# Kernel tuning notes

Measured on AMD Instinct MI355X. Metric: run time of the kernel, lower is better.

The kernel has to match this reference:

```python
import jax, jax.numpy as jnp
import numpy as np

NUM_EMBEDDINGS = 1024
EMBEDDING_DIM = 64


def setup_inputs() -> dict:
    key = jax.random.key(0)
    k1, k2 = jax.random.split(key)
    z = jax.random.normal(k1, (64, 32, 32, EMBEDDING_DIM), dtype=jnp.float32)
    # torch init: uniform_(-1/num_embeddings, 1/num_embeddings)
    lim = 1.0 / NUM_EMBEDDINGS
    codebook = jax.random.uniform(
        k2, (NUM_EMBEDDINGS, EMBEDDING_DIM), dtype=jnp.float32,
        minval=-lim, maxval=lim)
    return {"z": z, "codebook": codebook}


def reference(z, codebook):
    # z: [..., D]; codebook: [K, D]
    z_flat = z.reshape(-1, z.shape[-1])                      # [N, D]
    # ||z||^2 - 2 z.e + ||e||^2  -> [N, K]
    distances = (
        jnp.sum(z_flat ** 2, axis=1, keepdims=True)
        - 2.0 * jnp.einsum("nd,kd->nk", z_flat, codebook)
        + jnp.sum(codebook ** 2, axis=1)
    )
    min_indices = jnp.argmin(distances, axis=1)              # [N]
    z_q = jnp.take(codebook, min_indices, axis=0).reshape(z.shape)
    return z_q, min_indices
```

## Files before the change

### kernel.cpp

```cpp
#include <hip/hip_runtime.h>
#include <hip/hip_bf16.h>
#include <math.h>


#define D      64
#define K      1024
#define BLOCK  256

typedef _Float16 half8_t __attribute__((ext_vector_type(8)));
typedef float    floatx4 __attribute__((ext_vector_type(4)));

#define WS_CN_OFF    0
#define WS_EF_OFF    4096

__device__ __forceinline__ float np_sumsq64_p(const float* __restrict__ x) {
    float r[8];
    {
        float4 v0 = *(const float4*)(x);
        float4 v1 = *(const float4*)(x + 4);
        r[0] = __fmul_rn(v0.x, v0.x); r[1] = __fmul_rn(v0.y, v0.y);
        r[2] = __fmul_rn(v0.z, v0.z); r[3] = __fmul_rn(v0.w, v0.w);
        r[4] = __fmul_rn(v1.x, v1.x); r[5] = __fmul_rn(v1.y, v1.y);
        r[6] = __fmul_rn(v1.z, v1.z); r[7] = __fmul_rn(v1.w, v1.w);
    }
#pragma unroll
    for (int i = 8; i < 64; i += 8) {
        float4 v0 = *(const float4*)(x + i);
        float4 v1 = *(const float4*)(x + i + 4);
        r[0] = __fadd_rn(r[0], __fmul_rn(v0.x, v0.x));
        r[1] = __fadd_rn(r[1], __fmul_rn(v0.y, v0.y));
        r[2] = __fadd_rn(r[2], __fmul_rn(v0.z, v0.z));
        r[3] = __fadd_rn(r[3], __fmul_rn(v0.w, v0.w));
        r[4] = __fadd_rn(r[4], __fmul_rn(v1.x, v1.x));
        r[5] = __fadd_rn(r[5], __fmul_rn(v1.y, v1.y));
        r[6] = __fadd_rn(r[6], __fmul_rn(v1.z, v1.z));
        r[7] = __fadd_rn(r[7], __fmul_rn(v1.w, v1.w));
    }
    return __fadd_rn(__fadd_rn(__fadd_rn(r[0], r[1]), __fadd_rn(r[2], r[3])),
                     __fadd_rn(__fadd_rn(r[4], r[5]), __fadd_rn(r[6], r[7])));
}

__global__ void vq_pre(const float* __restrict__ cb, float* __restrict__ cn,
                       _Float16* __restrict__ ef) {
    const int k = blockIdx.x * 64 + threadIdx.x;
    if (k >= K) return;
    cn[k] = np_sumsq64_p(cb + (long)k * D);
    const int t = k >> 6, ct = (k >> 4) & 3, l16 = k & 15;
#pragma unroll
    for (int ch = 0; ch < 2; ++ch)
#pragma unroll
        for (int quad = 0; quad < 4; ++quad) {
            const float* p = cb + (long)k * D + ch * 32 + quad * 8;
            half8_t h1, h2;
#pragma unroll
            for (int j = 0; j < 8; ++j) {
                float x10 = __fmul_rn(p[j], 1024.0f);
                _Float16 g1 = (_Float16)x10;
                h1[j] = g1;
                h2[j] = (_Float16)(__fmul_rn(__fsub_rn(x10, (float)g1), 2048.0f));
            }
            const int base = t * 8192 + ct * 2048 + 128 * quad + 8 * l16;
            *(half8_t*)(ef + base + 512 * (ch))       = h1;
            *(half8_t*)(ef + base + 512 * (2 + ch))   = h2;
        }
}

__global__ __launch_bounds__(BLOCK, 2) void vq_main(
    const float* __restrict__ z, const float* __restrict__ cb,
    const _Float16* __restrict__ ef, const float* __restrict__ cn,
    float* __restrict__ zq, float* __restrict__ idx_out) {
    __shared__ __align__(16) float zf[128 * 68];
    __shared__ float sS[128];
    __shared__ float sCn[K];
    __shared__ int   sBi[128];

    const int tid  = threadIdx.x;
    const int lane = tid & 63;
    const int wv   = tid >> 6;
    const int quad = lane >> 4;
    const int l16  = lane & 15;
    const long rowbase = (long)blockIdx.x * 128;

    const float4* gz = (const float4*)(z + rowbase * D);
#pragma unroll
    for (int i = 0; i < 8; ++i) {
        int idx4 = i * BLOCK + tid;
        int r = idx4 >> 4, j = idx4 & 15;
        *(float4*)(zf + r * 68 + j * 4) = gz[idx4];
    }
#pragma unroll
    for (int i = 0; i < 4; ++i) sCn[i * 256 + tid] = cn[i * 256 + tid];
    __syncthreads();

    if (tid < 128) sS[tid] = np_sumsq64_p(zf + tid * 68);

    half8_t a1[2][2], a2[2][2];
#pragma unroll
    for (int rt = 0; rt < 2; ++rt) {
        const int row = wv * 32 + rt * 16 + l16;
#pragma unroll
        for (int ch = 0; ch < 2; ++ch) {
            const float* p = zf + row * 68 + ch * 32 + quad * 8;
            float4 f0 = *(const float4*)(p);
            float4 f1 = *(const float4*)(p + 4);
            float xs[8] = {f0.x, f0.y, f0.z, f0.w, f1.x, f1.y, f1.z, f1.w};
#pragma unroll
            for (int j = 0; j < 8; ++j) {
                _Float16 h1 = (_Float16)xs[j];
                a1[rt][ch][j] = h1;
                a2[rt][ch][j] =
                    (_Float16)(__fmul_rn(__fsub_rn(xs[j], (float)h1), 2048.0f));
            }
        }
    }
    __syncthreads();

    float myS[2][4];
#pragma unroll
    for (int rt = 0; rt < 2; ++rt)
#pragma unroll
        for (int r = 0; r < 4; ++r)
            myS[rt][r] = sS[wv * 32 + rt * 16 + quad * 4 + r];

    float bv[2][4];
    int   bi[2][4];
#pragma unroll
    for (int rt = 0; rt < 2; ++rt)
#pragma unroll
        for (int r = 0; r < 4; ++r) { bv[rt][r] = INFINITY; bi[rt][r] = 0; }

    const char* eb = (const char*)ef + 16 * lane;
    const floatx4 Z4g = {0.f, 0.f, 0.f, 0.f};

#define LOADG(b1_, b2_, g_) do {                                              \
        const char* p_ = eb + (size_t)(g_) * 4096;                            \
        b1_[0] = *(const half8_t*)(p_);                                       \
        b1_[1] = *(const half8_t*)(p_ + 1024);                                \
        b2_[0] = *(const half8_t*)(p_ + 2048);                                \
        b2_[1] = *(const half8_t*)(p_ + 3072);                                \
    } while (0)

#define COMPUTE(b1_, b2_, g_) do {                                            \
        const int   kg_  = (g_) * 16 + l16;                                   \
        const float cnv_ = sCn[kg_];                                          \
        floatx4 aM0, aM1, aC0, aC1;                                           \
        aM0 = __builtin_amdgcn_mfma_f32_16x16x32_f16(a1[0][0], b1_[0], Z4g, 0, 0, 0); \
        aM1 = __builtin_amdgcn_mfma_f32_16x16x32_f16(a1[1][0], b1_[0], Z4g, 0, 0, 0); \
        aM0 = __builtin_amdgcn_mfma_f32_16x16x32_f16(a1[0][1], b1_[1], aM0, 0, 0, 0); \
        aM1 = __builtin_amdgcn_mfma_f32_16x16x32_f16(a1[1][1], b1_[1], aM1, 0, 0, 0); \
        aC0 = __builtin_amdgcn_mfma_f32_16x16x32_f16(a1[0][0], b2_[0], Z4g, 0, 0, 0); \
        aC1 = __builtin_amdgcn_mfma_f32_16x16x32_f16(a1[1][0], b2_[0], Z4g, 0, 0, 0); \
        aC0 = __builtin_amdgcn_mfma_f32_16x16x32_f16(a1[0][1], b2_[1], aC0, 0, 0, 0); \
        aC1 = __builtin_amdgcn_mfma_f32_16x16x32_f16(a1[1][1], b2_[1], aC1, 0, 0, 0); \
        aC0 = __builtin_amdgcn_mfma_f32_16x16x32_f16(a2[0][0], b1_[0], aC0, 0, 0, 0); \
        aC1 = __builtin_amdgcn_mfma_f32_16x16x32_f16(a2[1][0], b1_[0], aC1, 0, 0, 0); \
        aC0 = __builtin_amdgcn_mfma_f32_16x16x32_f16(a2[0][1], b1_[1], aC0, 0, 0, 0); \
        aC1 = __builtin_amdgcn_mfma_f32_16x16x32_f16(a2[1][1], b1_[1], aC1, 0, 0, 0); \
        _Pragma("unroll")                                                     \
        for (int r = 0; r < 4; ++r) {                                         \
            float ds0 = fmaf(aC0[r], 0x1p-11f, aM0[r]);                       \
            float d0  = __fadd_rn(__fsub_rn(myS[0][r],                        \
                            __fmul_rn(ds0, 0x1p-9f)), cnv_);                  \
            if (d0 < bv[0][r]) { bv[0][r] = d0; bi[0][r] = kg_; }             \
            float ds1 = fmaf(aC1[r], 0x1p-11f, aM1[r]);                       \
            float d1  = __fadd_rn(__fsub_rn(myS[1][r],                        \
                            __fmul_rn(ds1, 0x1p-9f)), cnv_);                  \
            if (d1 < bv[1][r]) { bv[1][r] = d1; bi[1][r] = kg_; }             \
        }                                                                     \
    } while (0)

    half8_t b1A[2], b2A[2], b1B[2], b2B[2], b1C[2], b2C[2];
    LOADG(b1A, b2A, 0);
    LOADG(b1B, b2B, 1);
    for (int g = 0; g < 63; g += 3) {
        LOADG(b1C, b2C, g + 2);
        COMPUTE(b1A, b2A, g);
        if (g + 3 < 64) LOADG(b1A, b2A, g + 3);
        COMPUTE(b1B, b2B, g + 1);
        if (g + 4 < 64) LOADG(b1B, b2B, g + 4);
        COMPUTE(b1C, b2C, g + 2);
    }
    COMPUTE(b1A, b2A, 63);

#undef LOADG
#undef COMPUTE

#pragma unroll
    for (int rt = 0; rt < 2; ++rt)
#pragma unroll
        for (int r = 0; r < 4; ++r) {
            float v = bv[rt][r];
            int   x = bi[rt][r];
#pragma unroll
            for (int off = 1; off <= 8; off <<= 1) {
                float ov = __shfl_xor(v, off);
                int   ox = __shfl_xor(x, off);
                if (ov < v || (ov == v && ox < x)) { v = ov; x = ox; }
            }
            if (l16 == 0) {
                const int rl = wv * 32 + rt * 16 + quad * 4 + r;
                sBi[rl] = x;
                idx_out[rowbase + rl] = (float)x;
            }
        }
    __syncthreads();

    const float4* cb4 = (const float4*)cb;
    float4* zq4 = (float4*)(zq + rowbase * D);
#pragma unroll
    for (int i = 0; i < 8; ++i) {
        int idx4 = i * BLOCK + tid;
        int r = idx4 >> 4, j = idx4 & 15;
        zq4[idx4] = cb4[(long)sBi[r] * 16 + j];
    }
}

extern "C" void kernel_launch(void* const* d_in, const int* in_sizes, int n_in,
                              void* d_out, int out_size, void* d_ws, size_t ws_size,
                              hipStream_t stream) {
    const float* z  = (const float*)d_in[0];
    const float* cb = (const float*)d_in[1];

    const int n_rows = in_sizes[0] / D;
    float* zq      = (float*)d_out;
    float* idx_out = zq + (long)n_rows * D;

    float*    ws_cn = (float*)((char*)d_ws + WS_CN_OFF);
    _Float16* ws_ef = (_Float16*)((char*)d_ws + WS_EF_OFF);

    vq_pre<<<K / 64, 64, 0, stream>>>(cb, ws_cn, ws_ef);
    vq_main<<<n_rows / 128, BLOCK, 0, stream>>>(z, cb, ws_ef, ws_cn, zq, idx_out);
}
```

Before: 102.1 us.

## Prefetch codebook before z staging, shorten MFMA chains, prescale norms

Issues the first two codebook fragment loads before staging z into shared memory, so that global latency overlaps the prologue. Splits the correction MFMA accumulation into two independent chains (aC and aD), which shortens dependency depth. Prescales the z and codebook norms by 512 so one multiply per distance drops out. Parallelises the row sum-of-squares across 256 threads with a shuffle, and prefetches the codebook norm from shared memory alongside the fragments. Costs are higher register pressure and slightly different float rounding in the distance terms.

New measurement: 103.0 us. About the same (+0.8%).

```diff
diff --git a/kernel.cpp b/kernel.cpp
--- a/kernel.cpp
+++ b/kernel.cpp
@@ -81,58 +81,9 @@
     const int l16  = lane & 15;
     const long rowbase = (long)blockIdx.x * 128;
 
-    const float4* gz = (const float4*)(z + rowbase * D);
-#pragma unroll
-    for (int i = 0; i < 8; ++i) {
-        int idx4 = i * BLOCK + tid;
-        int r = idx4 >> 4, j = idx4 & 15;
-        *(float4*)(zf + r * 68 + j * 4) = gz[idx4];
-    }
-#pragma unroll
-    for (int i = 0; i < 4; ++i) sCn[i * 256 + tid] = cn[i * 256 + tid];
-    __syncthreads();
-
-    if (tid < 128) sS[tid] = np_sumsq64_p(zf + tid * 68);
-
-    half8_t a1[2][2], a2[2][2];
-#pragma unroll
-    for (int rt = 0; rt < 2; ++rt) {
-        const int row = wv * 32 + rt * 16 + l16;
-#pragma unroll
-        for (int ch = 0; ch < 2; ++ch) {
-            const float* p = zf + row * 68 + ch * 32 + quad * 8;
-            float4 f0 = *(const float4*)(p);
-            float4 f1 = *(const float4*)(p + 4);
-            float xs[8] = {f0.x, f0.y, f0.z, f0.w, f1.x, f1.y, f1.z, f1.w};
-#pragma unroll
-            for (int j = 0; j < 8; ++j) {
-                _Float16 h1 = (_Float16)xs[j];
-                a1[rt][ch][j] = h1;
-                a2[rt][ch][j] =
-                    (_Float16)(__fmul_rn(__fsub_rn(xs[j], (float)h1), 2048.0f));
-            }
-        }
-    }
-    __syncthreads();
-
-    float myS[2][4];
-#pragma unroll
-    for (int rt = 0; rt < 2; ++rt)
-#pragma unroll
-        for (int r = 0; r < 4; ++r)
-            myS[rt][r] = sS[wv * 32 + rt * 16 + quad * 4 + r];
-
-    float bv[2][4];
-    int   bi[2][4];
-#pragma unroll
-    for (int rt = 0; rt < 2; ++rt)
-#pragma unroll
-        for (int r = 0; r < 4; ++r) { bv[rt][r] = INFINITY; bi[rt][r] = 0; }
-
     const char* eb = (const char*)ef + 16 * lane;
-    const floatx4 Z4g = {0.f, 0.f, 0.f, 0.f};
-
-#define LOADG(b1_, b2_, g_) do {                                              \
+
+#define LOADB(b1_, b2_, g_) do {                                              \
         const char* p_ = eb + (size_t)(g_) * 4096;                            \
         b1_[0] = *(const half8_t*)(p_);                                       \
         b1_[1] = *(const half8_t*)(p_ + 1024);                                \
@@ -140,48 +91,129 @@
         b2_[1] = *(const half8_t*)(p_ + 3072);                                \
     } while (0)
 
-#define COMPUTE(b1_, b2_, g_) do {                                            \
-        const int   kg_  = (g_) * 16 + l16;                                   \
-        const float cnv_ = sCn[kg_];                                          \
-        floatx4 aM0, aM1, aC0, aC1;                                           \
+    half8_t b1A[2], b2A[2], b1B[2], b2B[2], b1C[2], b2C[2];
+    LOADB(b1A, b2A, 0);
+    LOADB(b1B, b2B, 1);
+
+    const float4* gz = (const float4*)(z + rowbase * D);
+#pragma unroll
+    for (int i = 0; i < 8; ++i) {
+        int idx4 = i * BLOCK + tid;
+        int r = idx4 >> 4, j = idx4 & 15;
+        *(float4*)(zf + r * 68 + j * 4) = gz[idx4];
+    }
+#pragma unroll
+    for (int i = 0; i < 4; ++i)
+        sCn[i * 256 + tid] = __fmul_rn(cn[i * 256 + tid], 512.0f);
+    __syncthreads();
+
+    {
+        const int row = tid >> 1, h = tid & 1;
+        const float* x = zf + row * 68 + 4 * h;
+        float r0, r1, r2, r3;
+        {
+            float4 v = *(const float4*)(x);
+            r0 = __fmul_rn(v.x, v.x); r1 = __fmul_rn(v.y, v.y);
+            r2 = __fmul_rn(v.z, v.z); r3 = __fmul_rn(v.w, v.w);
+        }
+#pragma unroll
+        for (int i = 8; i < 64; i += 8) {
+            float4 v = *(const float4*)(x + i);
+            r0 = __fadd_rn(r0, __fmul_rn(v.x, v.x));
+            r1 = __fadd_rn(r1, __fmul_rn(v.y, v.y));
+            r2 = __fadd_rn(r2, __fmul_rn(v.z, v.z));
+            r3 = __fadd_rn(r3, __fmul_rn(v.w, v.w));
+        }
+        float part = __fadd_rn(__fadd_rn(r0, r1), __fadd_rn(r2, r3));
+        float oth  = __shfl_xor(part, 1);
+        if (h == 0)
+            sS[row] = __fmul_rn(__fadd_rn(part, oth), 512.0f);
+    }
+
+    half8_t a1[2][2], a2[2][2];
+#pragma unroll
+    for (int rt = 0; rt < 2; ++rt) {
+        const int row = wv * 32 + rt * 16 + l16;
+#pragma unroll
+        for (int ch = 0; ch < 2; ++ch) {
+            const float* p = zf + row * 68 + ch * 32 + quad * 8;
+            float4 f0 = *(const float4*)(p);
+            float4 f1 = *(const float4*)(p + 4);
+            float xs[8] = {f0.x, f0.y, f0.z, f0.w, f1.x, f1.y, f1.z, f1.w};
+#pragma unroll
+            for (int j = 0; j < 8; ++j) {
+                _Float16 h1 = (_Float16)xs[j];
+                a1[rt][ch][j] = h1;
+                a2[rt][ch][j] =
+                    (_Float16)(__fmul_rn(__fsub_rn(xs[j], (float)h1), 2048.0f));
+            }
+        }
+    }
+    __syncthreads();
+
+    float myS9[2][4];
+#pragma unroll
+    for (int rt = 0; rt < 2; ++rt)
+#pragma unroll
+        for (int r = 0; r < 4; ++r)
+            myS9[rt][r] = sS[wv * 32 + rt * 16 + quad * 4 + r];
+
+    float bv[2][4];
+    int   bi[2][4];
+#pragma unroll
+    for (int rt = 0; rt < 2; ++rt)
+#pragma unroll
+        for (int r = 0; r < 4; ++r) { bv[rt][r] = INFINITY; bi[rt][r] = 0; }
+
+    const floatx4 Z4g = {0.f, 0.f, 0.f, 0.f};
+
+#define COMPUTE(b1_, b2_, cn9_, g_) do {                                      \
+        const int kg_ = (g_) * 16 + l16;                                      \
+        floatx4 aM0, aM1, aC0, aC1, aD0, aD1;                                 \
         aM0 = __builtin_amdgcn_mfma_f32_16x16x32_f16(a1[0][0], b1_[0], Z4g, 0, 0, 0); \
         aM1 = __builtin_amdgcn_mfma_f32_16x16x32_f16(a1[1][0], b1_[0], Z4g, 0, 0, 0); \
+        aC0 = __builtin_amdgcn_mfma_f32_16x16x32_f16(a1[0][0], b2_[0], Z4g, 0, 0, 0); \
+        aC1 = __builtin_amdgcn_mfma_f32_16x16x32_f16(a1[1][0], b2_[0], Z4g, 0, 0, 0); \
+        aD0 = __builtin_amdgcn_mfma_f32_16x16x32_f16(a2[0][0], b1_[0], Z4g, 0, 0, 0); \
+        aD1 = __builtin_amdgcn_mfma_f32_16x16x32_f16(a2[1][0], b1_[0], Z4g, 0, 0, 0); \
         aM0 = __builtin_amdgcn_mfma_f32_16x16x32_f16(a1[0][1], b1_[1], aM0, 0, 0, 0); \
         aM1 = __builtin_amdgcn_mfma_f32_16x16x32_f16(a1[1][1], b1_[1], aM1, 0, 0, 0); \
-        aC0 = __builtin_amdgcn_mfma_f32_16x16x32_f16(a1[0][0], b2_[0], Z4g, 0, 0, 0); \
-        aC1 = __builtin_amdgcn_mfma_f32_16x16x32_f16(a1[1][0], b2_[0], Z4g, 0, 0, 0); \
         aC0 = __builtin_amdgcn_mfma_f32_16x16x32_f16(a1[0][1], b2_[1], aC0, 0, 0, 0); \
         aC1 = __builtin_amdgcn_mfma_f32_16x16x32_f16(a1[1][1], b2_[1], aC1, 0, 0, 0); \
-        aC0 = __builtin_amdgcn_mfma_f32_16x16x32_f16(a2[0][0], b1_[0], aC0, 0, 0, 0); \
-        aC1 = __builtin_amdgcn_mfma_f32_16x16x32_f16(a2[1][0], b1_[0], aC1, 0, 0, 0); \
-        aC0 = __builtin_amdgcn_mfma_f32_16x16x32_f16(a2[0][1], b1_[1], aC0, 0, 0, 0); \
-        aC1 = __builtin_amdgcn_mfma_f32_16x16x32_f16(a2[1][1], b1_[1], aC1, 0, 0, 0); \
+        aD0 = __builtin_amdgcn_mfma_f32_16x16x32_f16(a2[0][1], b1_[1], aD0, 0, 0, 0); \
+        aD1 = __builtin_amdgcn_mfma_f32_16x16x32_f16(a2[1][1], b1_[1], aD1, 0, 0, 0); \
         _Pragma("unroll")                                                     \
         for (int r = 0; r < 4; ++r) {                                         \
-            float ds0 = fmaf(aC0[r], 0x1p-11f, aM0[r]);                       \
-            float d0  = __fadd_rn(__fsub_rn(myS[0][r],                        \
-                            __fmul_rn(ds0, 0x1p-9f)), cnv_);                  \
+            float sc0 = __fadd_rn(aC0[r], aD0[r]);                            \
+            float ds0 = fmaf(sc0, 0x1p-11f, aM0[r]);                          \
+            float d0  = __fadd_rn(__fsub_rn(myS9[0][r], ds0), cn9_);          \
             if (d0 < bv[0][r]) { bv[0][r] = d0; bi[0][r] = kg_; }             \
-            float ds1 = fmaf(aC1[r], 0x1p-11f, aM1[r]);                       \
-            float d1  = __fadd_rn(__fsub_rn(myS[1][r],                        \
-                            __fmul_rn(ds1, 0x1p-9f)), cnv_);                  \
+            float sc1 = __fadd_rn(aC1[r], aD1[r]);                            \
+            float ds1 = fmaf(sc1, 0x1p-11f, aM1[r]);                          \
+            float d1  = __fadd_rn(__fsub_rn(myS9[1][r], ds1), cn9_);          \
             if (d1 < bv[1][r]) { bv[1][r] = d1; bi[1][r] = kg_; }             \
         }                                                                     \
     } while (0)
 
-    half8_t b1A[2], b2A[2], b1B[2], b2B[2], b1C[2], b2C[2];
-    LOADG(b1A, b2A, 0);
-    LOADG(b1B, b2B, 1);
+#define LOADG(b1_, b2_, cn9_, g_) do {                                        \
+        LOADB(b1_, b2_, g_);                                                  \
+        cn9_ = sCn[(g_) * 16 + l16];                                          \
+    } while (0)
+
+    float cnA, cnB, cnC;
+    cnA = sCn[0 * 16 + l16];
+    cnB = sCn[1 * 16 + l16];
     for (int g = 0; g < 63; g += 3) {
-        LOADG(b1C, b2C, g + 2);
-        COMPUTE(b1A, b2A, g);
-        if (g + 3 < 64) LOADG(b1A, b2A, g + 3);
-        COMPUTE(b1B, b2B, g + 1);
-        if (g + 4 < 64) LOADG(b1B, b2B, g + 4);
-        COMPUTE(b1C, b2C, g + 2);
-    }
-    COMPUTE(b1A, b2A, 63);
-
+        LOADG(b1C, b2C, cnC, g + 2);
+        COMPUTE(b1A, b2A, cnA, g);
+        if (g + 3 < 64) LOADG(b1A, b2A, cnA, g + 3);
+        COMPUTE(b1B, b2B, cnB, g + 1);
+        if (g + 4 < 64) LOADG(b1B, b2B, cnB, g + 4);
+        COMPUTE(b1C, b2C, cnC, g + 2);
+    }
+    COMPUTE(b1A, b2A, cnA, 63);
+
+#undef LOADB
 #undef LOADG
 #undef COMPUTE
 
```
